# Kernel tuning notes

Hardware: AMD Instinct MI355X
Metric: run time of the kernel (lower is better)

The kernel has to match this reference:

```python
import jax, jax.numpy as jnp
import numpy as np

N = 10000
E = 160000
IN_DIM = 128
OUT_DIM = 32
HEADS = 32
H1 = OUT_DIM * 2   # 64 per-head channels in layer 1
H2 = OUT_DIM       # 32 per-head channels in layer 2
NEG_SLOPE = 0.2
EPS = 1e-16  # PyG softmax denominator epsilon


def gat_layer(x, src, dst, W, a_src, a_dst, b, n_nodes, heads, ch):
    # x: [N, F_in], W: [F_in, heads*ch], a_src/a_dst: [heads, ch], b: [ch]
    xp = (x @ W).reshape(n_nodes, heads, ch)                 # [N,H,C]
    alpha_s = jnp.einsum('nhc,hc->nh', xp, a_src)            # [N,H]
    alpha_d = jnp.einsum('nhc,hc->nh', xp, a_dst)            # [N,H]
    e = jax.nn.leaky_relu(alpha_s[src] + alpha_d[dst], NEG_SLOPE)  # [E,H]
    # segment softmax over edges grouped by destination node
    m = jax.ops.segment_max(e, dst, num_segments=n_nodes)    # [N,H]
    e = jnp.exp(e - m[dst])                                  # [E,H]
    s = jax.ops.segment_sum(e, dst, num_segments=n_nodes)    # [N,H]
    alpha = e / (s[dst] + EPS)                               # [E,H]
    msg = alpha[:, :, None] * xp[src]                        # [E,H,C]
    out = jax.ops.segment_sum(msg, dst, num_segments=n_nodes)  # [N,H,C]
    return out.mean(axis=1) + b                              # concat=False: head mean, [N,C]


def setup_inputs() -> dict:
    key = jax.random.key(0)
    ks = jax.random.split(key, 9)
    x = jax.random.normal(ks[0], (N, IN_DIM), dtype=jnp.float32)
    edge_index = jax.random.randint(ks[1], (2, E), 0, N, dtype=jnp.int64)
    W1 = jax.random.normal(ks[2], (IN_DIM, HEADS * H1), dtype=jnp.float32) * 0.1
    a_src1 = jax.random.normal(ks[3], (HEADS, H1), dtype=jnp.float32) * 0.1
    a_dst1 = jax.random.normal(ks[4], (HEADS, H1), dtype=jnp.float32) * 0.1
    b1 = jnp.zeros((H1,), dtype=jnp.float32)
    W2 = jax.random.normal(ks[5], (H1, HEADS * H2), dtype=jnp.float32) * 0.1
    a_src2 = jax.random.normal(ks[6], (HEADS, H2), dtype=jnp.float32) * 0.1
    a_dst2 = jax.random.normal(ks[7], (HEADS, H2), dtype=jnp.float32) * 0.1
    b2 = jnp.zeros((H2,), dtype=jnp.float32)
    return {"x": x, "edge_index": edge_index,
            "W1": W1, "a_src1": a_src1, "a_dst1": a_dst1, "b1": b1,
            "W2": W2, "a_src2": a_src2, "a_dst2": a_dst2, "b2": b2}


def reference(x, edge_index, W1, a_src1, a_dst1, b1, W2, a_src2, a_dst2, b2):
    # flow='source_to_target': messages go edge_index[0] -> edge_index[1]
    src = edge_index[0]
    dst = edge_index[1]
    z1 = jax.nn.elu(gat_layer(x, src, dst, W1, a_src1, a_dst1, b1, N, HEADS, H1))
    z2 = jax.nn.elu(gat_layer(z1, src, dst, W2, a_src2, a_dst2, b2, N, HEADS, H2))
    return jnp.concatenate((z1, z2), axis=-1)  # [N, 96]
```

## Files before the change

kernel.cpp:

```cpp
#include <hip/hip_runtime.h>
#include <hip/hip_bf16.h>

#define NN 10000
#define NE 160000
#define NH 32
#define LRELU_SLOPE 0.2f
#define SM_EPS 1e-16f
#define SM_SHIFT 16.0f

typedef __hip_bfloat16 bf16;
typedef __attribute__((ext_vector_type(8))) __bf16 bf16x8;
typedef __attribute__((ext_vector_type(4))) float f32x4;

__device__ __forceinline__ float bits2f(unsigned int u16) {
    union { unsigned int u; float f; } v; v.u = u16 << 16; return v.f;
}
__device__ __forceinline__ void loadbf8(const bf16* __restrict__ p, float f[8]) {
    uint4 v = *reinterpret_cast<const uint4*>(p);
    f[0] = bits2f(v.x & 0xffffu); f[1] = bits2f(v.x >> 16);
    f[2] = bits2f(v.y & 0xffffu); f[3] = bits2f(v.y >> 16);
    f[4] = bits2f(v.z & 0xffffu); f[5] = bits2f(v.z >> 16);
    f[6] = bits2f(v.w & 0xffffu); f[7] = bits2f(v.w >> 16);
}

__global__ void k_edge_detect(const unsigned int* __restrict__ raw, int* __restrict__ flag) {
    if (threadIdx.x == 0 && blockIdx.x == 0) {
        int z = 1;
        for (int i = 1; i < 32; i += 2) z &= (raw[i] == 0u);
        *flag = z;
    }
}
__global__ void k_edge_norm(const int* __restrict__ raw, const int* __restrict__ flag,
                            int* __restrict__ srcv, int* __restrict__ dstv, int* __restrict__ deg) {
    int e = blockIdx.x * blockDim.x + threadIdx.x;
    if (e < NN) deg[e] = 0;
    if (e >= NE) return;
    if (*flag) { srcv[e] = raw[2 * e]; dstv[e] = raw[2 * (NE + e)]; }
    else       { srcv[e] = raw[e];     dstv[e] = raw[NE + e]; }
}

__global__ void k_hist(const int* __restrict__ dstv, int* __restrict__ deg) {
    int e = blockIdx.x * blockDim.x + threadIdx.x;
    if (e < NE) atomicAdd(&deg[dstv[e]], 1);
}
__global__ void k_scan(const int* __restrict__ deg, int* __restrict__ offs, int* __restrict__ cursor) {
    __shared__ int wsum[16], wpre[16];
    __shared__ int base;
    const int tid = threadIdx.x, lane = tid & 63, wid = tid >> 6;
    if (tid == 0) base = 0;
    __syncthreads();
    for (int chunk = 0; chunk < NN; chunk += 1024) {
        int idx = chunk + tid;
        int v = (idx < NN) ? deg[idx] : 0;
        int s = v;
        #pragma unroll
        for (int off = 1; off < 64; off <<= 1) {
            int t = __shfl_up(s, off);
            if (lane >= off) s += t;
        }
        if (lane == 63) wsum[wid] = s;
        __syncthreads();
        if (wid == 0) {
            int ws = (lane < 16) ? wsum[lane] : 0;
            #pragma unroll
            for (int off = 1; off < 16; off <<= 1) {
                int t = __shfl_up(ws, off);
                if (lane >= off) ws += t;
            }
            if (lane < 16) wpre[lane] = ws;
        }
        __syncthreads();
        int wbase = (wid == 0) ? 0 : wpre[wid - 1];
        int excl = base + wbase + s - v;
        if (idx < NN) { offs[idx] = excl; cursor[idx] = excl; }
        int total = wpre[15];
        __syncthreads();
        if (tid == 0) base += total;
        __syncthreads();
    }
    if (tid == 0) offs[NN] = base;
}
__global__ void k_scatter(const int* __restrict__ srcv, const int* __restrict__ dstv,
                          int* __restrict__ cursor, int* __restrict__ srcs) {
    int e = blockIdx.x * blockDim.x + threadIdx.x;
    if (e < NE) {
        int p = atomicAdd(&cursor[dstv[e]], 1);
        srcs[p] = srcv[e];
    }
}

__global__ void k_prep(const float* __restrict__ X, bf16* __restrict__ Xb,
                       const float* __restrict__ W1, bf16* __restrict__ Wt1,
                       const float* __restrict__ W2, bf16* __restrict__ Wt2) {
    int i = blockIdx.x * blockDim.x + threadIdx.x;
    if (i < NN * 128) { Xb[i] = __float2bfloat16(X[i]); return; }
    i -= NN * 128;
    if (i < 128 * 2048) {
        int k = i / 2048, m = i - k * 2048;
        Wt1[(size_t)m * 128 + k] = __float2bfloat16(W1[i]);
        return;
    }
    i -= 128 * 2048;
    if (i < 64 * 1024) {
        int k = i / 1024, m = i - k * 1024;
        Wt2[(size_t)m * 64 + k] = __float2bfloat16(W2[i]);
    }
}

template<int K, int M, int C>
__global__ __launch_bounds__(256) void k_gemm_mfma(
        const bf16* __restrict__ Xb, const bf16* __restrict__ Wt,
        const float* __restrict__ Asrc, const float* __restrict__ Adst,
        bf16* __restrict__ XPB, float* __restrict__ aS, float* __restrict__ aD) {
    constexpr int BM = 64, BN = 128;
    constexpr int KB = K * 2;
    constexpr int NHB = BN / C;
    constexpr int WPH = C / 32;
    __shared__ char lds[(BM + BN) * KB];
    __shared__ float sredS[4][BM], sredD[4][BM];
    char* lA = lds;
    char* lB = lds + BM * KB;

    const int tid = threadIdx.x;
    const int wv = tid >> 6, ln = tid & 63;
    const int lrow = ln & 15, lkb = ln >> 4;
    const int brow = blockIdx.x * BM;
    const int bcol = blockIdx.y * BN;

    #pragma unroll
    for (int c = 0; c < BM * K / 8 / 256; c++) {
        int it = c * 256 + tid;
        int r = it / (K / 8), kc = (it % (K / 8)) * 8;
        int node = brow + r;
        uint4 v = make_uint4(0u, 0u, 0u, 0u);
        if (node < NN) v = *reinterpret_cast<const uint4*>(&Xb[(size_t)node * K + kc]);
        *reinterpret_cast<uint4*>(lA + ((r * KB + kc * 2) ^ ((r & 7) << 4))) = v;
    }
    #pragma unroll
    for (int c = 0; c < BN * K / 8 / 256; c++) {
        int it = c * 256 + tid;
        int r = it / (K / 8), kc = (it % (K / 8)) * 8;
        uint4 v = *reinterpret_cast<const uint4*>(&Wt[(size_t)(bcol + r) * K + kc]);
        *reinterpret_cast<uint4*>(lB + ((r * KB + kc * 2) ^ ((r & 7) << 4))) = v;
    }
    __syncthreads();

    f32x4 acc[4][2];
    #pragma unroll
    for (int mi = 0; mi < 4; mi++)
        #pragma unroll
        for (int nj = 0; nj < 2; nj++) acc[mi][nj] = (f32x4){0.f, 0.f, 0.f, 0.f};

    #pragma unroll
    for (int ks = 0; ks < K / 32; ks++) {
        const int k0 = ks * 32 + lkb * 8;
        bf16x8 af[4], bfr[2];
        #pragma unroll
        for (int mi = 0; mi < 4; mi++) {
            int r = mi * 16 + lrow;
            af[mi] = *reinterpret_cast<const bf16x8*>(lA + ((r * KB + k0 * 2) ^ ((r & 7) << 4)));
        }
        #pragma unroll
        for (int nj = 0; nj < 2; nj++) {
            int r = wv * 32 + nj * 16 + lrow;
            bfr[nj] = *reinterpret_cast<const bf16x8*>(lB + ((r * KB + k0 * 2) ^ ((r & 7) << 4)));
        }
        #pragma unroll
        for (int mi = 0; mi < 4; mi++)
            #pragma unroll
            for (int nj = 0; nj < 2; nj++)
                acc[mi][nj] = __builtin_amdgcn_mfma_f32_16x16x32_bf16(af[mi], bfr[nj], acc[mi][nj], 0, 0, 0);
    }

    float ar0 = Asrc[bcol + wv * 32 + lrow];
    float ar1 = Asrc[bcol + wv * 32 + 16 + lrow];
    float ad0 = Adst[bcol + wv * 32 + lrow];
    float ad1 = Adst[bcol + wv * 32 + 16 + lrow];

    #pragma unroll
    for (int mi = 0; mi < 4; mi++) {
        #pragma unroll
        for (int r = 0; r < 4; r++) {
            int rowl = mi * 16 + lkb * 4 + r;
            int row = brow + rowl;
            if (row < NN) {
                XPB[(size_t)row * M + bcol + wv * 32 + lrow]      = __float2bfloat16(acc[mi][0][r]);
                XPB[(size_t)row * M + bcol + wv * 32 + 16 + lrow] = __float2bfloat16(acc[mi][1][r]);
            }
            float vs = acc[mi][0][r] * ar0 + acc[mi][1][r] * ar1;
            float vd = acc[mi][0][r] * ad0 + acc[mi][1][r] * ad1;
            vs += __shfl_xor(vs, 1); vd += __shfl_xor(vd, 1);
            vs += __shfl_xor(vs, 2); vd += __shfl_xor(vd, 2);
            vs += __shfl_xor(vs, 4); vd += __shfl_xor(vd, 4);
            vs += __shfl_xor(vs, 8); vd += __shfl_xor(vd, 8);
            if (lrow == 0) {
                sredS[wv][rowl] = vs;
                sredD[wv][rowl] = vd;
            }
        }
    }
    __syncthreads();
    if (tid < BM) {
        int node = brow + tid;
        if (node < NN) {
            #pragma unroll
            for (int hb = 0; hb < NHB; hb++) {
                float ss = 0.f, dd = 0.f;
                #pragma unroll
                for (int w = 0; w < WPH; w++) {
                    ss += sredS[hb * WPH + w][tid];
                    dd += sredD[hb * WPH + w][tid];
                }
                int h = bcol / C + hb;
                aS[node * NH + h] = ss;
                aD[node * NH + h] = dd;
            }
        }
    }
}

template<int C, bool WZ>
__global__ void k_agg_fused(const bf16* __restrict__ XPB,
                            const float* __restrict__ aS, const float* __restrict__ aD,
                            const int* __restrict__ offs, const int* __restrict__ srcs,
                            const float* __restrict__ bias, float* __restrict__ out, int col0,
                            bf16* __restrict__ z1b) {
    const int M = NH * C;
    const int tid = threadIdx.x;
    const int node = blockIdx.x;
    const int m0 = tid * 8;
    const int h = m0 / C;
    const int beg = offs[node], end = offs[node + 1];
    const float ad = aD[node * NH + h];
    float acc[8];
    #pragma unroll
    for (int j = 0; j < 8; j++) acc[j] = 0.f;
    float ssum = 0.f;
    int i = beg;
    for (; i + 4 <= end; i += 4) {
        int s0 = srcs[i], s1 = srcs[i + 1], s2 = srcs[i + 2], s3 = srcs[i + 3];
        float c0 = aS[s0 * NH + h] + ad;
        float c1 = aS[s1 * NH + h] + ad;
        float c2 = aS[s2 * NH + h] + ad;
        float c3 = aS[s3 * NH + h] + ad;
        c0 = (c0 >= 0.f) ? c0 : LRELU_SLOPE * c0;
        c1 = (c1 >= 0.f) ? c1 : LRELU_SLOPE * c1;
        c2 = (c2 >= 0.f) ? c2 : LRELU_SLOPE * c2;
        c3 = (c3 >= 0.f) ? c3 : LRELU_SLOPE * c3;
        float p0 = expf(c0 - SM_SHIFT), p1 = expf(c1 - SM_SHIFT);
        float p2 = expf(c2 - SM_SHIFT), p3 = expf(c3 - SM_SHIFT);
        ssum += (p0 + p1) + (p2 + p3);
        float x0[8], x1[8], x2[8], x3[8];
        loadbf8(&XPB[(size_t)s0 * M + m0], x0);
        loadbf8(&XPB[(size_t)s1 * M + m0], x1);
        loadbf8(&XPB[(size_t)s2 * M + m0], x2);
        loadbf8(&XPB[(size_t)s3 * M + m0], x3);
        #pragma unroll
        for (int j = 0; j < 8; j++) {
            acc[j] = fmaf(p0, x0[j], acc[j]);
            acc[j] = fmaf(p1, x1[j], acc[j]);
            acc[j] = fmaf(p2, x2[j], acc[j]);
            acc[j] = fmaf(p3, x3[j], acc[j]);
        }
    }
    for (; i < end; i++) {
        int s = srcs[i];
        float c = aS[s * NH + h] + ad;
        c = (c >= 0.f) ? c : LRELU_SLOPE * c;
        float p = expf(c - SM_SHIFT);
        ssum += p;
        float xv[8];
        loadbf8(&XPB[(size_t)s * M + m0], xv);
        #pragma unroll
        for (int j = 0; j < 8; j++) acc[j] = fmaf(p, xv[j], acc[j]);
    }
    float r = 1.f / (ssum + SM_EPS);
    __shared__ float red[NH * C];
    #pragma unroll
    for (int j = 0; j < 8; j++) red[m0 + j] = acc[j] * r;
    __syncthreads();
    if (tid < C) {
        float sres = 0.f;
        #pragma unroll 8
        for (int hh = 0; hh < NH; hh++) sres += red[hh * C + tid];
        sres = sres * (1.0f / NH) + bias[tid];
        sres = (sres > 0.f) ? sres : expm1f(sres);
        out[(size_t)node * 96 + col0 + tid] = sres;
        if constexpr (WZ) z1b[(size_t)node * C + tid] = __float2bfloat16(sres);
    }
}

extern "C" void kernel_launch(void* const* d_in, const int* in_sizes, int n_in,
                              void* d_out, int out_size, void* d_ws, size_t ws_size,
                              hipStream_t stream) {
    const float* x   = (const float*)d_in[0];
    const int*   ei  = (const int*)d_in[1];
    const float* W1  = (const float*)d_in[2];
    const float* as1 = (const float*)d_in[3];
    const float* ad1 = (const float*)d_in[4];
    const float* b1  = (const float*)d_in[5];
    const float* W2  = (const float*)d_in[6];
    const float* as2 = (const float*)d_in[7];
    const float* ad2 = (const float*)d_in[8];
    const float* b2  = (const float*)d_in[9];
    float* out = (float*)d_out;

    char* w = (char*)d_ws;
    size_t off = 0;
    auto alloc = [&](size_t bytes) -> void* {
        void* p = w + off;
        off = (off + bytes + 255) & ~(size_t)255;
        return p;
    };
    bf16*  xpb    = (bf16*)alloc((size_t)NN * 2048 * 2);
    float* aS     = (float*)alloc((size_t)NN * NH * 4);
    float* aD     = (float*)alloc((size_t)NN * NH * 4);
    int*   deg    = (int*)alloc((size_t)NN * 4);
    int*   cursor = (int*)alloc((size_t)NN * 4);
    int*   offs   = (int*)alloc((size_t)(NN + 1) * 4);
    int*   srcs   = (int*)alloc((size_t)NE * 4);
    int*   srcv   = (int*)alloc((size_t)NE * 4);
    int*   dstv   = (int*)alloc((size_t)NE * 4);
    bf16*  Xb     = (bf16*)alloc((size_t)NN * 128 * 2);
    bf16*  Wt1    = (bf16*)alloc((size_t)2048 * 128 * 2);
    bf16*  Wt2    = (bf16*)alloc((size_t)1024 * 64 * 2);
    bf16*  z1b    = (bf16*)alloc((size_t)NN * 64 * 2);
    int*   eflag  = (int*)alloc(256);
    (void)ws_size; (void)in_sizes; (void)n_in; (void)out_size;

    k_edge_detect<<<1, 64, 0, stream>>>((const unsigned int*)ei, eflag);
    k_edge_norm<<<(NE + 255) / 256, 256, 0, stream>>>(ei, eflag, srcv, dstv, deg);
    k_hist<<<NE / 256, 256, 0, stream>>>(dstv, deg);
    k_scan<<<1, 1024, 0, stream>>>(deg, offs, cursor);
    k_scatter<<<NE / 256, 256, 0, stream>>>(srcv, dstv, cursor, srcs);

    k_prep<<<(NN * 128 + 128 * 2048 + 64 * 1024 + 255) / 256, 256, 0, stream>>>(
        x, Xb, W1, Wt1, W2, Wt2);

    k_gemm_mfma<128, 2048, 64><<<dim3((NN + 63) / 64, 2048 / 128), 256, 0, stream>>>(
        Xb, Wt1, as1, ad1, xpb, aS, aD);
    k_agg_fused<64, true><<<NN, 256, 0, stream>>>(xpb, aS, aD, offs, srcs, b1, out, 0, z1b);

    k_gemm_mfma<64, 1024, 32><<<dim3((NN + 63) / 64, 1024 / 128), 256, 0, stream>>>(
        z1b, Wt2, as2, ad2, xpb, aS, aD);
    k_agg_fused<32, false><<<NN, 128, 0, stream>>>(xpb, aS, aD, offs, srcs, b2, out, 64, nullptr);
}
```

Baseline: 232.0 us.

## Split aggregation into per-slice edge-parallel kernels with partial-sum reduce

Replaces the one-block-per-node aggregation with a kernel in which each wavefront handles one node for a 128-column slice (a group of heads), and four edge lanes split the edge list and are combined with cross-lane shuffles. Slice blockIdx ordering keeps the same column slice of XPB hot in cache across neighbouring nodes, and the head mean is done by a separate reduce kernel over fp32 partials. The aim is better cache locality and parallelism over edges. In exchange it writes and reads large partial buffers and adds kernel launches. It also switches to the fast __expf.

Result: slower. 252.6 us (+8.9%).

```diff
diff --git a/kernel.cpp b/kernel.cpp
--- a/kernel.cpp
+++ b/kernel.cpp
@@ -219,75 +219,74 @@
     }
 }
 
-template<int C, bool WZ>
-__global__ void k_agg_fused(const bf16* __restrict__ XPB,
-                            const float* __restrict__ aS, const float* __restrict__ aD,
-                            const int* __restrict__ offs, const int* __restrict__ srcs,
-                            const float* __restrict__ bias, float* __restrict__ out, int col0,
-                            bf16* __restrict__ z1b) {
-    const int M = NH * C;
-    const int tid = threadIdx.x;
-    const int node = blockIdx.x;
-    const int m0 = tid * 8;
-    const int h = m0 / C;
+template<int C>
+__global__ __launch_bounds__(256) void k_agg_slice(
+        const bf16* __restrict__ XPB, const float* __restrict__ aS,
+        const float* __restrict__ aD, const int* __restrict__ offs,
+        const int* __restrict__ srcs, float* __restrict__ P, int sg0) {
+    constexpr int M = NH * C;
+    constexpr int HPS = 128 / C;
+    constexpr int CGH = C / 8;
+    const int sg = sg0 + (blockIdx.x & 7);
+    const int wid = threadIdx.x >> 6, lane = threadIdx.x & 63;
+    const int node = (blockIdx.x >> 3) * 4 + wid;
+    const int cg = lane & 15, el = lane >> 4;
+    const int hl = cg / CGH;
+    const int h = sg * HPS + hl;
+    const int col = sg * 128 + cg * 8;
     const int beg = offs[node], end = offs[node + 1];
     const float ad = aD[node * NH + h];
     float acc[8];
     #pragma unroll
     for (int j = 0; j < 8; j++) acc[j] = 0.f;
     float ssum = 0.f;
-    int i = beg;
-    for (; i + 4 <= end; i += 4) {
-        int s0 = srcs[i], s1 = srcs[i + 1], s2 = srcs[i + 2], s3 = srcs[i + 3];
-        float c0 = aS[s0 * NH + h] + ad;
-        float c1 = aS[s1 * NH + h] + ad;
-        float c2 = aS[s2 * NH + h] + ad;
-        float c3 = aS[s3 * NH + h] + ad;
-        c0 = (c0 >= 0.f) ? c0 : LRELU_SLOPE * c0;
-        c1 = (c1 >= 0.f) ? c1 : LRELU_SLOPE * c1;
-        c2 = (c2 >= 0.f) ? c2 : LRELU_SLOPE * c2;
-        c3 = (c3 >= 0.f) ? c3 : LRELU_SLOPE * c3;
-        float p0 = expf(c0 - SM_SHIFT), p1 = expf(c1 - SM_SHIFT);
-        float p2 = expf(c2 - SM_SHIFT), p3 = expf(c3 - SM_SHIFT);
-        ssum += (p0 + p1) + (p2 + p3);
-        float x0[8], x1[8], x2[8], x3[8];
-        loadbf8(&XPB[(size_t)s0 * M + m0], x0);
-        loadbf8(&XPB[(size_t)s1 * M + m0], x1);
-        loadbf8(&XPB[(size_t)s2 * M + m0], x2);
-        loadbf8(&XPB[(size_t)s3 * M + m0], x3);
-        #pragma unroll
-        for (int j = 0; j < 8; j++) {
-            acc[j] = fmaf(p0, x0[j], acc[j]);
-            acc[j] = fmaf(p1, x1[j], acc[j]);
-            acc[j] = fmaf(p2, x2[j], acc[j]);
-            acc[j] = fmaf(p3, x3[j], acc[j]);
-        }
-    }
-    for (; i < end; i++) {
+    for (int i = beg + el; i < end; i += 4) {
         int s = srcs[i];
-        float c = aS[s * NH + h] + ad;
-        c = (c >= 0.f) ? c : LRELU_SLOPE * c;
-        float p = expf(c - SM_SHIFT);
+        float sc = aS[s * NH + h] + ad;
+        sc = (sc >= 0.f) ? sc : LRELU_SLOPE * sc;
+        float p = __expf(sc - SM_SHIFT);
         ssum += p;
         float xv[8];
-        loadbf8(&XPB[(size_t)s * M + m0], xv);
+        loadbf8(&XPB[(size_t)s * M + col], xv);
         #pragma unroll
         for (int j = 0; j < 8; j++) acc[j] = fmaf(p, xv[j], acc[j]);
     }
+    #pragma unroll
+    for (int j = 0; j < 8; j++) {
+        acc[j] += __shfl_xor(acc[j], 16);
+        acc[j] += __shfl_xor(acc[j], 32);
+    }
+    ssum += __shfl_xor(ssum, 16);
+    ssum += __shfl_xor(ssum, 32);
     float r = 1.f / (ssum + SM_EPS);
-    __shared__ float red[NH * C];
-    #pragma unroll
-    for (int j = 0; j < 8; j++) red[m0 + j] = acc[j] * r;
-    __syncthreads();
-    if (tid < C) {
-        float sres = 0.f;
-        #pragma unroll 8
-        for (int hh = 0; hh < NH; hh++) sres += red[hh * C + tid];
-        sres = sres * (1.0f / NH) + bias[tid];
-        sres = (sres > 0.f) ? sres : expm1f(sres);
-        out[(size_t)node * 96 + col0 + tid] = sres;
-        if constexpr (WZ) z1b[(size_t)node * C + tid] = __float2bfloat16(sres);
-    }
+    #pragma unroll
+    for (int j = 0; j < 8; j++) acc[j] *= r;
+    #pragma unroll
+    for (int j = 0; j < 8; j++) acc[j] += __shfl_xor(acc[j], 8);
+    if constexpr (HPS == 4) {
+        #pragma unroll
+        for (int j = 0; j < 8; j++) acc[j] += __shfl_xor(acc[j], 4);
+    }
+    if (el == 0 && cg < CGH) {
+        float* dst = &P[((size_t)sg * NN + node) * C + cg * 8];
+        *reinterpret_cast<float4*>(dst)     = make_float4(acc[0], acc[1], acc[2], acc[3]);
+        *reinterpret_cast<float4*>(dst + 4) = make_float4(acc[4], acc[5], acc[6], acc[7]);
+    }
+}
+
+template<int C, int NS, bool WZ>
+__global__ void k_reduce(const float* __restrict__ P, const float* __restrict__ bias,
+                         float* __restrict__ out, int col0, bf16* __restrict__ z1b) {
+    const int tid = threadIdx.x;
+    const int node = blockIdx.x * (256 / C) + tid / C;
+    const int c = tid % C;
+    float s = 0.f;
+    #pragma unroll
+    for (int sg = 0; sg < NS; sg++) s += P[((size_t)sg * NN + node) * C + c];
+    s = s * (1.0f / NH) + bias[c];
+    s = (s > 0.f) ? s : expm1f(s);
+    out[(size_t)node * 96 + col0 + c] = s;
+    if constexpr (WZ) z1b[(size_t)node * C + c] = __float2bfloat16(s);
 }
 
 extern "C" void kernel_launch(void* const* d_in, const int* in_sizes, int n_in,
@@ -315,6 +314,8 @@
     bf16*  xpb    = (bf16*)alloc((size_t)NN * 2048 * 2);
     float* aS     = (float*)alloc((size_t)NN * NH * 4);
     float* aD     = (float*)alloc((size_t)NN * NH * 4);
+    float* P1     = (float*)alloc((size_t)16 * NN * 64 * 4);
+    float* P2     = (float*)alloc((size_t)8 * NN * 32 * 4);
     int*   deg    = (int*)alloc((size_t)NN * 4);
     int*   cursor = (int*)alloc((size_t)NN * 4);
     int*   offs   = (int*)alloc((size_t)(NN + 1) * 4);
@@ -339,9 +340,12 @@
 
     k_gemm_mfma<128, 2048, 64><<<dim3((NN + 63) / 64, 2048 / 128), 256, 0, stream>>>(
         Xb, Wt1, as1, ad1, xpb, aS, aD);
-    k_agg_fused<64, true><<<NN, 256, 0, stream>>>(xpb, aS, aD, offs, srcs, b1, out, 0, z1b);
+    k_agg_slice<64><<<(NN / 4) * 8, 256, 0, stream>>>(xpb, aS, aD, offs, srcs, P1, 0);
+    k_agg_slice<64><<<(NN / 4) * 8, 256, 0, stream>>>(xpb, aS, aD, offs, srcs, P1, 8);
+    k_reduce<64, 16, true><<<NN / 4, 256, 0, stream>>>(P1, b1, out, 0, z1b);
 
     k_gemm_mfma<64, 1024, 32><<<dim3((NN + 63) / 64, 1024 / 128), 256, 0, stream>>>(
         z1b, Wt2, as2, ad2, xpb, aS, aD);
-    k_agg_fused<32, false><<<NN, 128, 0, stream>>>(xpb, aS, aD, offs, srcs, b2, out, 64, nullptr);
-}
+    k_agg_slice<32><<<(NN / 4) * 8, 256, 0, stream>>>(xpb, aS, aD, offs, srcs, P2, 0);
+    k_reduce<32, 8, false><<<NN / 8, 256, 0, stream>>>(P2, b2, out, 64, nullptr);
+}
```
